# Optimization experiments

Measured on AMD Instinct MI355X. Metric: run time of the kernel, lower is better.

The kernel has to match this reference:

```python
import jax, jax.numpy as jnp
import numpy as np
from jax import lax

B = 32768

def setup_inputs() -> dict:
    key = jax.random.key(0)
    ks = jax.random.split(key, 8)
    return {
        "x": jax.random.normal(ks[0], (B, 784), dtype=jnp.float32),
        "w_conv": jax.random.normal(ks[1], (3, 3), dtype=jnp.float32),
        "W1": jax.random.normal(ks[2], (676, 100), dtype=jnp.float32) * 0.05,
        "b1": jax.random.normal(ks[3], (100,), dtype=jnp.float32) * 0.05,
        "W2": jax.random.normal(ks[4], (100, 100), dtype=jnp.float32) * 0.05,
        "b2": jax.random.normal(ks[5], (100,), dtype=jnp.float32) * 0.05,
        "W3": jax.random.normal(ks[6], (100, 10), dtype=jnp.float32) * 0.05,
        "b3": jax.random.normal(ks[7], (10,), dtype=jnp.float32) * 0.05,
    }


def reference(x, w_conv, W1, b1, W2, b2, W3, b3):
    # x: [B, 784] -> [B, 1, 28, 28]; valid 3x3 cross-correlation (tensordot == correlation)
    xr = x.reshape(-1, 1, 28, 28)
    k = w_conv.reshape(1, 1, 3, 3)  # [out_c, in_c, kh, kw]
    conv = lax.conv_general_dilated(
        xr, k, window_strides=(1, 1), padding="VALID",
        dimension_numbers=("NCHW", "OIHW", "NCHW"))  # [B, 1, 26, 26]
    h = conv.reshape(conv.shape[0], 26 * 26)  # [B, 676]
    h = jax.nn.relu(h @ W1 + b1)
    h = jax.nn.relu(h @ W2 + b2)
    return h @ W3 + b3  # [B, 10]
```

## Files before the change

kernel.cpp:

```cpp
#include <hip/hip_runtime.h>


typedef __attribute__((ext_vector_type(8))) short bf16x8;
typedef __attribute__((ext_vector_type(4))) float f32x4;

#define KP1 832
#define NP  112
#define K2P 128
#define BM  64
#define NT  256

#define W2T_OFF (NP * KP1)
#define W3T_OFF (W2T_OFF + NP * K2P)
#define WS_USHORTS (W3T_OFF + 16 * K2P)

#define WAITV4 asm volatile("s_waitcnt vmcnt(4)" ::: "memory")
#define WAITV0 asm volatile("s_waitcnt vmcnt(0)" ::: "memory")
#define BAR    __builtin_amdgcn_s_barrier()
#define SBAR0  __builtin_amdgcn_sched_barrier(0)

__device__ __forceinline__ unsigned short f2bf(float f) {
    unsigned int u = __float_as_uint(f);
    u += 0x7FFFu + ((u >> 16) & 1u);
    return (unsigned short)(u >> 16);
}

__device__ __forceinline__ unsigned int pkbf(float a, float b) {
    unsigned int r;
    asm("v_cvt_pk_bf16_f32 %0, %1, %2" : "=v"(r) : "v"(a), "v"(b));
    return r;
}

__device__ __forceinline__ bf16x8 cvt8(float4 a, float4 b) {
    union { unsigned int w[4]; bf16x8 v; } u;
    u.w[0] = pkbf(a.x, a.y);
    u.w[1] = pkbf(a.z, a.w);
    u.w[2] = pkbf(b.x, b.y);
    u.w[3] = pkbf(b.z, b.w);
    return u.v;
}

__device__ __forceinline__ void gload_lds16(const void* g, void* l) {
    __builtin_amdgcn_global_load_lds(
        (const __attribute__((address_space(1))) unsigned int*)g,
        (__attribute__((address_space(3))) unsigned int*)l, 16, 0, 0);
}

__global__ void build_weights(const float* __restrict__ w_conv,
                              const float* __restrict__ W1,
                              const float* __restrict__ W2,
                              const float* __restrict__ W3,
                              unsigned short* __restrict__ ws) {
    const int idx = blockIdx.x * 256 + threadIdx.x;
    const int WEFF_T = 28 * KP1;
    if (idx < WEFF_T) {
        const int j4 = idx / KP1, p = idx % KP1;
        const int j = j4 * 4;
        float a0 = 0.f, a1 = 0.f, a2 = 0.f, a3 = 0.f;
        if (p < 784 && j4 < 25) {
            const int y = p / 28, xx = p % 28;
#pragma unroll
            for (int ky = 0; ky < 3; ++ky) {
                const int py = y - ky;
                if (py < 0 || py >= 26) continue;
#pragma unroll
                for (int kx = 0; kx < 3; ++kx) {
                    const int px = xx - kx;
                    if (px < 0 || px >= 26) continue;
                    const float wc = w_conv[ky * 3 + kx];
                    const float4 w = *reinterpret_cast<const float4*>(
                        W1 + (size_t)(py * 26 + px) * 100 + j);
                    a0 = fmaf(wc, w.x, a0); a1 = fmaf(wc, w.y, a1);
                    a2 = fmaf(wc, w.z, a2); a3 = fmaf(wc, w.w, a3);
                }
            }
        }
        ws[(size_t)(j + 0) * KP1 + p] = f2bf(a0);
        ws[(size_t)(j + 1) * KP1 + p] = f2bf(a1);
        ws[(size_t)(j + 2) * KP1 + p] = f2bf(a2);
        ws[(size_t)(j + 3) * KP1 + p] = f2bf(a3);
    } else if (idx < WEFF_T + NP * K2P) {
        const int r = idx - WEFF_T;
        const int col = r / K2P, k = r % K2P;
        float v = (col < 100 && k < 100) ? W2[k * 100 + col] : 0.f;
        ws[W2T_OFF + r] = f2bf(v);
    } else if (idx < WEFF_T + NP * K2P + 16 * K2P) {
        const int r = idx - WEFF_T - NP * K2P;
        const int col = r / K2P, k = r % K2P;
        float v = (col < 10 && k < 100) ? W3[k * 10 + col] : 0.f;
        ws[W3T_OFF + r] = f2bf(v);
    }
}

__global__ __launch_bounds__(NT, 2)
void fused(const float* __restrict__ x,
           const unsigned short* __restrict__ wst,
           const float* __restrict__ b1,
           const float* __restrict__ b2,
           const float* __restrict__ b3,
           float* __restrict__ out) {
    __shared__ __attribute__((aligned(16))) float          xs[3][64][64];
    __shared__ __attribute__((aligned(16))) unsigned short bs[2][112][64];
    unsigned short (*h1)[136] = reinterpret_cast<unsigned short(*)[136]>(&xs[0][0][0]);
    unsigned short (*h2)[136] = reinterpret_cast<unsigned short(*)[136]>(
        (char*)&xs[0][0][0] + 17408);

    const int tid  = threadIdx.x;
    const int lane = tid & 63;
    const int wv   = tid >> 6;
    const int l15  = lane & 15;
    const int lk   = lane >> 4;
    const int b0   = blockIdx.x * BM;
    const int wr   = wv * 16;

    const unsigned short* weff = wst;
    const unsigned short* w2t  = wst + W2T_OFF;
    const unsigned short* w3t  = wst + W3T_OFF;

    f32x4 acc[7];
#pragma unroll
    for (int n = 0; n < 7; ++n) acc[n] = (f32x4){0.f, 0.f, 0.f, 0.f};

    auto issueX = [&](int kt, float* xb) {
#pragma unroll
        for (int q = 0; q < 4; ++q) {
            const int rowbase = wr + 4 * q;
            const int r = rowbase + (lane >> 4);
            const int chunk = (lane & 15) ^ (r & 7);
            const char* g = (const char*)(x + (size_t)(b0 + r) * 784 + kt * 64)
                          + chunk * 16;
            gload_lds16(g, (char*)xb + rowbase * 256);
        }
    };
    auto issueB = [&](int kt, unsigned short* bb) {
#pragma unroll
        for (int k = 0; k < 4; ++k) {
            const int i = wv + 4 * k;
            if (i < 14) {
                const int rowbase = 8 * i;
                const int r = rowbase + (lane >> 3);
                const int chunk = (lane & 7) ^ (r & 7);
                const char* g = (const char*)(weff + (size_t)r * KP1 + kt * 64)
                              + chunk * 16;
                gload_lds16(g, (char*)bb + rowbase * 128);
            }
        }
    };

    auto computeStage = [&](const float* xb, const unsigned short* bb) {
        const int r = wr + l15;
        const int sA = (r & 7) << 4;
        const char* ap = (const char*)xb + r * 256;
#pragma unroll
        for (int ks = 0; ks < 2; ++ks) {
            const int base = ks * 128 + lk * 32;
            const float4 lo = *reinterpret_cast<const float4*>(ap + ((base     ) ^ sA));
            const float4 hi = *reinterpret_cast<const float4*>(ap + ((base + 16) ^ sA));
            const bf16x8 af = cvt8(lo, hi);
#pragma unroll
            for (int n = 0; n < 7; ++n) {
                const int rn = n * 16 + l15;
                const char* bp = (const char*)bb + rn * 128;
                const bf16x8 bfr = *reinterpret_cast<const bf16x8*>(
                    bp + ((ks * 64 + lk * 16) ^ ((rn & 7) << 4)));
                acc[n] = __builtin_amdgcn_mfma_f32_16x16x32_bf16(af, bfr, acc[n], 0, 0, 0);
            }
        }
    };

    float*          X[3] = {&xs[0][0][0], &xs[1][0][0], &xs[2][0][0]};
    unsigned short* Bf[2] = {&bs[0][0][0], &bs[1][0][0]};

    issueX(0, X[0]); issueB(0, Bf[0]); issueX(1, X[1]);
    WAITV4; BAR;
#pragma unroll
    for (int t = 0; t < 12; ++t) {
        if (t < 11) issueB(t + 1, Bf[(t + 1) & 1]);
        if (t < 10) issueX(t + 2, X[(t + 2) % 3]);
        SBAR0;
        computeStage(X[t % 3], Bf[t & 1]);
        if (t < 10)      { WAITV4; BAR; }
        else if (t == 10){ WAITV0; BAR; }
    }

    {
        float4 t0 = (float4){0.f, 0.f, 0.f, 0.f}, t1 = t0;
        if (lk < 2) {
            const float* xp = x + (size_t)(b0 + wr + l15) * 784 + 768 + lk * 8;
            t0 = *reinterpret_cast<const float4*>(xp);
            t1 = *reinterpret_cast<const float4*>(xp + 4);
        }
        const bf16x8 aft = cvt8(t0, t1);
#pragma unroll
        for (int n = 0; n < 7; ++n) {
            const bf16x8 bft = *reinterpret_cast<const bf16x8*>(
                weff + (size_t)(n * 16 + l15) * KP1 + 768 + lk * 8);
            acc[n] = __builtin_amdgcn_mfma_f32_16x16x32_bf16(aft, bft, acc[n], 0, 0, 0);
        }
    }
    __syncthreads();

    float bias[7];
#pragma unroll
    for (int n = 0; n < 7; ++n) {
        const int c = n * 16 + l15;
        bias[n] = (c < 100) ? b1[c] : 0.f;
    }
#pragma unroll
    for (int n = 0; n < 7; ++n) {
        const int col = n * 16 + l15;
        if (col < 100)
#pragma unroll
            for (int q = 0; q < 4; ++q) {
                const float v = fmaxf(acc[n][q] + bias[n], 0.f);
                h1[wr + lk * 4 + q][col] = f2bf(v);
            }
    }
    for (int f = lane; f < 16 * 14; f += 64) {
        const int r = wr + f / 14, c = 100 + (f % 14) * 2;
        *reinterpret_cast<unsigned int*>(&h1[r][c]) = 0u;
        *reinterpret_cast<unsigned int*>(&h2[r][c]) = 0u;
    }
    SBAR0;

    f32x4 acc2[7];
#pragma unroll
    for (int n = 0; n < 7; ++n) acc2[n] = (f32x4){0.f, 0.f, 0.f, 0.f};
#pragma unroll
    for (int ks = 0; ks < 4; ++ks) {
        const int kb = ks * 32 + lk * 8;
        const bf16x8 af = *reinterpret_cast<const bf16x8*>(&h1[wr + l15][kb]);
#pragma unroll
        for (int n = 0; n < 7; ++n) {
            const bf16x8 bfr = *reinterpret_cast<const bf16x8*>(
                w2t + (size_t)(n * 16 + l15) * K2P + kb);
            acc2[n] = __builtin_amdgcn_mfma_f32_16x16x32_bf16(af, bfr, acc2[n], 0, 0, 0);
        }
    }

#pragma unroll
    for (int n = 0; n < 7; ++n) {
        const int c = n * 16 + l15;
        bias[n] = (c < 100) ? b2[c] : 0.f;
    }
#pragma unroll
    for (int n = 0; n < 7; ++n) {
        const int col = n * 16 + l15;
        if (col < 100)
#pragma unroll
            for (int q = 0; q < 4; ++q) {
                const float v = fmaxf(acc2[n][q] + bias[n], 0.f);
                h2[wr + lk * 4 + q][col] = f2bf(v);
            }
    }
    SBAR0;

    f32x4 acc3 = (f32x4){0.f, 0.f, 0.f, 0.f};
#pragma unroll
    for (int ks = 0; ks < 4; ++ks) {
        const int kb = ks * 32 + lk * 8;
        const bf16x8 bfr = *reinterpret_cast<const bf16x8*>(
            w3t + (size_t)l15 * K2P + kb);
        const bf16x8 af = *reinterpret_cast<const bf16x8*>(&h2[wr + l15][kb]);
        acc3 = __builtin_amdgcn_mfma_f32_16x16x32_bf16(af, bfr, acc3, 0, 0, 0);
    }

    if (l15 < 10) {
        const float bb = b3[l15];
#pragma unroll
        for (int q = 0; q < 4; ++q) {
            const int row = b0 + wr + lk * 4 + q;
            out[(size_t)row * 10 + l15] = acc3[q] + bb;
        }
    }
}

extern "C" void kernel_launch(void* const* d_in, const int* in_sizes, int n_in,
                              void* d_out, int out_size, void* d_ws, size_t ws_size,
                              hipStream_t stream) {
    const float* x      = (const float*)d_in[0];
    const float* w_conv = (const float*)d_in[1];
    const float* W1     = (const float*)d_in[2];
    const float* b1     = (const float*)d_in[3];
    const float* W2     = (const float*)d_in[4];
    const float* b2     = (const float*)d_in[5];
    const float* W3     = (const float*)d_in[6];
    const float* b3     = (const float*)d_in[7];
    float* out = (float*)d_out;
    unsigned short* ws = (unsigned short*)d_ws;

    const int total = 28 * KP1 + NP * K2P + 16 * K2P;
    build_weights<<<(total + 255) / 256, 256, 0, stream>>>(w_conv, W1, W2, W3, ws);
    fused<<<32768 / BM, NT, 0, stream>>>(x, ws, b1, b2, b3, out);
}
```

Before: 36.47 us.

## Warp-specialize fused MLP with copy waves converting x to bf16 in LDS

Splits each 512-thread block into four compute waves and four copy waves that stream 32-row tiles of x into a double-buffered bf16 LDS tile, overlapping the next tile's load with the current tile's three GEMMs. Each block handles four tiles, and first-layer weights are now read directly from global memory into registers rather than staged through LDS. This removes the fp32 LDS staging and per-step conversions. It risks lower memory-level parallelism from synchronous loads on only four waves and one block per CU due to large LDS use.

```diff
diff --git a/kernel.cpp b/kernel.cpp
--- a/kernel.cpp
+++ b/kernel.cpp
@@ -7,17 +7,15 @@
 #define KP1 832
 #define NP  112
 #define K2P 128
-#define BM  64
-#define NT  256
+#define NT  512
+#define TILES 4
+#define ROWS 32
+#define XC  840
 
 #define W2T_OFF (NP * KP1)
 #define W3T_OFF (W2T_OFF + NP * K2P)
-#define WS_USHORTS (W3T_OFF + 16 * K2P)
-
-#define WAITV4 asm volatile("s_waitcnt vmcnt(4)" ::: "memory")
-#define WAITV0 asm volatile("s_waitcnt vmcnt(0)" ::: "memory")
-#define BAR    __builtin_amdgcn_s_barrier()
-#define SBAR0  __builtin_amdgcn_sched_barrier(0)
+
+#define SBAR0 __builtin_amdgcn_sched_barrier(0)
 
 __device__ __forceinline__ unsigned short f2bf(float f) {
     unsigned int u = __float_as_uint(f);
@@ -29,21 +27,6 @@
     unsigned int r;
     asm("v_cvt_pk_bf16_f32 %0, %1, %2" : "=v"(r) : "v"(a), "v"(b));
     return r;
-}
-
-__device__ __forceinline__ bf16x8 cvt8(float4 a, float4 b) {
-    union { unsigned int w[4]; bf16x8 v; } u;
-    u.w[0] = pkbf(a.x, a.y);
-    u.w[1] = pkbf(a.z, a.w);
-    u.w[2] = pkbf(b.x, b.y);
-    u.w[3] = pkbf(b.z, b.w);
-    return u.v;
-}
-
-__device__ __forceinline__ void gload_lds16(const void* g, void* l) {
-    __builtin_amdgcn_global_load_lds(
-        (const __attribute__((address_space(1))) unsigned int*)g,
-        (__attribute__((address_space(3))) unsigned int*)l, 16, 0, 0);
 }
 
 __global__ void build_weights(const float* __restrict__ w_conv,
@@ -99,178 +82,177 @@
            const float* __restrict__ b2,
            const float* __restrict__ b3,
            float* __restrict__ out) {
-    __shared__ __attribute__((aligned(16))) float          xs[3][64][64];
-    __shared__ __attribute__((aligned(16))) unsigned short bs[2][112][64];
-    unsigned short (*h1)[136] = reinterpret_cast<unsigned short(*)[136]>(&xs[0][0][0]);
-    unsigned short (*h2)[136] = reinterpret_cast<unsigned short(*)[136]>(
-        (char*)&xs[0][0][0] + 17408);
+    __shared__ __attribute__((aligned(16))) unsigned short xs[2][ROWS][XC];
+    __shared__ __attribute__((aligned(16))) unsigned short h1[ROWS][136];
+    __shared__ __attribute__((aligned(16))) unsigned short h2[ROWS][136];
 
     const int tid  = threadIdx.x;
     const int lane = tid & 63;
     const int wv   = tid >> 6;
+    const bool is_copy = (wv >= 4);
     const int l15  = lane & 15;
     const int lk   = lane >> 4;
-    const int b0   = blockIdx.x * BM;
-    const int wr   = wv * 16;
+    const int wv_m = (wv >> 1) & 1;
+    const int wv_n = wv & 1;
+    const int wr   = wv_m * 16;
+    const int nb   = wv_n * 4;
+    const size_t b0 = (size_t)blockIdx.x * (TILES * ROWS);
 
     const unsigned short* weff = wst;
     const unsigned short* w2t  = wst + W2T_OFF;
     const unsigned short* w3t  = wst + W3T_OFF;
 
-    f32x4 acc[7];
-#pragma unroll
-    for (int n = 0; n < 7; ++n) acc[n] = (f32x4){0.f, 0.f, 0.f, 0.f};
-
-    auto issueX = [&](int kt, float* xb) {
-#pragma unroll
-        for (int q = 0; q < 4; ++q) {
-            const int rowbase = wr + 4 * q;
-            const int r = rowbase + (lane >> 4);
-            const int chunk = (lane & 15) ^ (r & 7);
-            const char* g = (const char*)(x + (size_t)(b0 + r) * 784 + kt * 64)
-                          + chunk * 16;
-            gload_lds16(g, (char*)xb + rowbase * 256);
+    for (int i = tid; i < 1536; i += NT) {
+        const int buf = i / 768, r = (i % 768) / 24, c = (i % 768) % 24;
+        *reinterpret_cast<unsigned int*>(&xs[buf][r][784 + c * 2]) = 0u;
+    }
+    for (int i = tid; i < 1152; i += NT) {
+        const int a = i / 576, r = (i % 576) / 18, c = (i % 576) % 18;
+        unsigned short* hp = a ? &h2[0][0] : &h1[0][0];
+        *reinterpret_cast<unsigned int*>(hp + r * 136 + 100 + c * 2) = 0u;
+    }
+    {
+        const float* src = x + b0 * 784;
+#pragma unroll
+        for (int i = 0; i < 13; ++i) {
+            const int f = i * 2048 + tid * 4;
+            if (f < ROWS * 784) {
+                const float4 v = *reinterpret_cast<const float4*>(src + f);
+                const int row = f / 784, col = f - row * 784;
+                *reinterpret_cast<uint2*>(&xs[0][row][col]) =
+                    (uint2){pkbf(v.x, v.y), pkbf(v.z, v.w)};
+            }
+        }
+    }
+    __syncthreads();
+
+    float bias1[4], bias2[4], bb3 = 0.f;
+    const unsigned short* bp[4];
+    if (!is_copy) {
+#pragma unroll
+        for (int j = 0; j < 4; ++j) {
+            const int nf = nb + j, c = nf * 16 + l15;
+            bias1[j] = (nf < 7 && c < 100) ? b1[c] : 0.f;
+            bias2[j] = (nf < 7 && c < 100) ? b2[c] : 0.f;
+            bp[j] = weff + (size_t)(nf * 16 + l15) * KP1;
+        }
+        if (wv_n == 0 && l15 < 10) bb3 = b3[l15];
+    }
+
+    auto copy_half = [&](int t1, int i0, int i1) {
+        const int ctid = tid - 256;
+        const float* src = x + (b0 + (size_t)t1 * ROWS) * 784;
+        unsigned short* dst = &xs[t1 & 1][0][0];
+#pragma unroll
+        for (int i = i0; i < i1; ++i) {
+            const int f = i * 1024 + ctid * 4;
+            if (f < ROWS * 784) {
+                const float4 v = *reinterpret_cast<const float4*>(src + f);
+                const int row = f / 784, col = f - row * 784;
+                *reinterpret_cast<uint2*>(dst + row * XC + col) =
+                    (uint2){pkbf(v.x, v.y), pkbf(v.z, v.w)};
+            }
         }
     };
-    auto issueB = [&](int kt, unsigned short* bb) {
-#pragma unroll
-        for (int k = 0; k < 4; ++k) {
-            const int i = wv + 4 * k;
-            if (i < 14) {
-                const int rowbase = 8 * i;
-                const int r = rowbase + (lane >> 3);
-                const int chunk = (lane & 7) ^ (r & 7);
-                const char* g = (const char*)(weff + (size_t)r * KP1 + kt * 64)
-                              + chunk * 16;
-                gload_lds16(g, (char*)bb + rowbase * 128);
-            }
-        }
-    };
-
-    auto computeStage = [&](const float* xb, const unsigned short* bb) {
-        const int r = wr + l15;
-        const int sA = (r & 7) << 4;
-        const char* ap = (const char*)xb + r * 256;
-#pragma unroll
-        for (int ks = 0; ks < 2; ++ks) {
-            const int base = ks * 128 + lk * 32;
-            const float4 lo = *reinterpret_cast<const float4*>(ap + ((base     ) ^ sA));
-            const float4 hi = *reinterpret_cast<const float4*>(ap + ((base + 16) ^ sA));
-            const bf16x8 af = cvt8(lo, hi);
-#pragma unroll
-            for (int n = 0; n < 7; ++n) {
-                const int rn = n * 16 + l15;
-                const char* bp = (const char*)bb + rn * 128;
+
+#pragma unroll 1
+    for (int t = 0; t < TILES; ++t) {
+        const unsigned short* xb = &xs[t & 1][0][0];
+
+        if (is_copy) {
+            if (t + 1 < TILES) copy_half(t + 1, 0, 13);
+        } else {
+            f32x4 acc[4];
+#pragma unroll
+            for (int j = 0; j < 4; ++j) acc[j] = (f32x4){0.f, 0.f, 0.f, 0.f};
+
+            bf16x8 A[2][2];
+            bf16x8 Bv[2][4][2];
+            const unsigned short* ap = xb + (wr + l15) * XC;
+
+            auto loadW = [&](int w, int b) {
+                A[b][0] = *reinterpret_cast<const bf16x8*>(ap + w * 64 + lk * 8);
+                A[b][1] = *reinterpret_cast<const bf16x8*>(ap + w * 64 + 32 + lk * 8);
+#pragma unroll
+                for (int j = 0; j < 4; ++j)
+                    if (nb + j < 7) {
+                        Bv[b][j][0] = *reinterpret_cast<const bf16x8*>(bp[j] + w * 64 + lk * 8);
+                        Bv[b][j][1] = *reinterpret_cast<const bf16x8*>(bp[j] + w * 64 + 32 + lk * 8);
+                    }
+            };
+            loadW(0, 0);
+#pragma unroll
+            for (int w = 0; w < 13; ++w) {
+                if (w < 12) loadW(w + 1, (w + 1) & 1);
+                SBAR0;
+#pragma unroll
+                for (int ks = 0; ks < 2; ++ks)
+#pragma unroll
+                    for (int j = 0; j < 4; ++j)
+                        if (nb + j < 7)
+                            acc[j] = __builtin_amdgcn_mfma_f32_16x16x32_bf16(
+                                A[w & 1][ks], Bv[w & 1][j][ks], acc[j], 0, 0, 0);
+                SBAR0;
+            }
+#pragma unroll
+            for (int j = 0; j < 4; ++j) {
+                const int nf = nb + j, col = nf * 16 + l15;
+                if (nf < 7 && col < 100)
+#pragma unroll
+                    for (int q = 0; q < 4; ++q)
+                        h1[wr + lk * 4 + q][col] = f2bf(fmaxf(acc[j][q] + bias1[j], 0.f));
+            }
+        }
+        __syncthreads();
+
+        if (is_copy) {
+            if (t + 1 < TILES) copy_half(t + 1, 13, 25);
+        } else {
+            f32x4 acc2[4];
+#pragma unroll
+            for (int j = 0; j < 4; ++j) acc2[j] = (f32x4){0.f, 0.f, 0.f, 0.f};
+#pragma unroll
+            for (int ks = 0; ks < 4; ++ks) {
+                const int kb = ks * 32 + lk * 8;
+                const bf16x8 af = *reinterpret_cast<const bf16x8*>(&h1[wr + l15][kb]);
+#pragma unroll
+                for (int j = 0; j < 4; ++j) {
+                    const int nf = nb + j;
+                    if (nf < 7) {
+                        const bf16x8 bfr = *reinterpret_cast<const bf16x8*>(
+                            w2t + (size_t)(nf * 16 + l15) * K2P + kb);
+                        acc2[j] = __builtin_amdgcn_mfma_f32_16x16x32_bf16(af, bfr, acc2[j], 0, 0, 0);
+                    }
+                }
+            }
+#pragma unroll
+            for (int j = 0; j < 4; ++j) {
+                const int nf = nb + j, col = nf * 16 + l15;
+                if (nf < 7 && col < 100)
+#pragma unroll
+                    for (int q = 0; q < 4; ++q)
+                        h2[wr + lk * 4 + q][col] = f2bf(fmaxf(acc2[j][q] + bias2[j], 0.f));
+            }
+        }
+        __syncthreads();
+
+        if (!is_copy && wv_n == 0) {
+            f32x4 acc3 = (f32x4){0.f, 0.f, 0.f, 0.f};
+#pragma unroll
+            for (int ks = 0; ks < 4; ++ks) {
+                const int kb = ks * 32 + lk * 8;
                 const bf16x8 bfr = *reinterpret_cast<const bf16x8*>(
-                    bp + ((ks * 64 + lk * 16) ^ ((rn & 7) << 4)));
-                acc[n] = __builtin_amdgcn_mfma_f32_16x16x32_bf16(af, bfr, acc[n], 0, 0, 0);
-            }
-        }
-    };
-
-    float*          X[3] = {&xs[0][0][0], &xs[1][0][0], &xs[2][0][0]};
-    unsigned short* Bf[2] = {&bs[0][0][0], &bs[1][0][0]};
-
-    issueX(0, X[0]); issueB(0, Bf[0]); issueX(1, X[1]);
-    WAITV4; BAR;
-#pragma unroll
-    for (int t = 0; t < 12; ++t) {
-        if (t < 11) issueB(t + 1, Bf[(t + 1) & 1]);
-        if (t < 10) issueX(t + 2, X[(t + 2) % 3]);
-        SBAR0;
-        computeStage(X[t % 3], Bf[t & 1]);
-        if (t < 10)      { WAITV4; BAR; }
-        else if (t == 10){ WAITV0; BAR; }
-    }
-
-    {
-        float4 t0 = (float4){0.f, 0.f, 0.f, 0.f}, t1 = t0;
-        if (lk < 2) {
-            const float* xp = x + (size_t)(b0 + wr + l15) * 784 + 768 + lk * 8;
-            t0 = *reinterpret_cast<const float4*>(xp);
-            t1 = *reinterpret_cast<const float4*>(xp + 4);
-        }
-        const bf16x8 aft = cvt8(t0, t1);
-#pragma unroll
-        for (int n = 0; n < 7; ++n) {
-            const bf16x8 bft = *reinterpret_cast<const bf16x8*>(
-                weff + (size_t)(n * 16 + l15) * KP1 + 768 + lk * 8);
-            acc[n] = __builtin_amdgcn_mfma_f32_16x16x32_bf16(aft, bft, acc[n], 0, 0, 0);
-        }
-    }
-    __syncthreads();
-
-    float bias[7];
-#pragma unroll
-    for (int n = 0; n < 7; ++n) {
-        const int c = n * 16 + l15;
-        bias[n] = (c < 100) ? b1[c] : 0.f;
-    }
-#pragma unroll
-    for (int n = 0; n < 7; ++n) {
-        const int col = n * 16 + l15;
-        if (col < 100)
-#pragma unroll
-            for (int q = 0; q < 4; ++q) {
-                const float v = fmaxf(acc[n][q] + bias[n], 0.f);
-                h1[wr + lk * 4 + q][col] = f2bf(v);
-            }
-    }
-    for (int f = lane; f < 16 * 14; f += 64) {
-        const int r = wr + f / 14, c = 100 + (f % 14) * 2;
-        *reinterpret_cast<unsigned int*>(&h1[r][c]) = 0u;
-        *reinterpret_cast<unsigned int*>(&h2[r][c]) = 0u;
-    }
-    SBAR0;
-
-    f32x4 acc2[7];
-#pragma unroll
-    for (int n = 0; n < 7; ++n) acc2[n] = (f32x4){0.f, 0.f, 0.f, 0.f};
-#pragma unroll
-    for (int ks = 0; ks < 4; ++ks) {
-        const int kb = ks * 32 + lk * 8;
-        const bf16x8 af = *reinterpret_cast<const bf16x8*>(&h1[wr + l15][kb]);
-#pragma unroll
-        for (int n = 0; n < 7; ++n) {
-            const bf16x8 bfr = *reinterpret_cast<const bf16x8*>(
-                w2t + (size_t)(n * 16 + l15) * K2P + kb);
-            acc2[n] = __builtin_amdgcn_mfma_f32_16x16x32_bf16(af, bfr, acc2[n], 0, 0, 0);
-        }
-    }
-
-#pragma unroll
-    for (int n = 0; n < 7; ++n) {
-        const int c = n * 16 + l15;
-        bias[n] = (c < 100) ? b2[c] : 0.f;
-    }
-#pragma unroll
-    for (int n = 0; n < 7; ++n) {
-        const int col = n * 16 + l15;
-        if (col < 100)
-#pragma unroll
-            for (int q = 0; q < 4; ++q) {
-                const float v = fmaxf(acc2[n][q] + bias[n], 0.f);
-                h2[wr + lk * 4 + q][col] = f2bf(v);
-            }
-    }
-    SBAR0;
-
-    f32x4 acc3 = (f32x4){0.f, 0.f, 0.f, 0.f};
-#pragma unroll
-    for (int ks = 0; ks < 4; ++ks) {
-        const int kb = ks * 32 + lk * 8;
-        const bf16x8 bfr = *reinterpret_cast<const bf16x8*>(
-            w3t + (size_t)l15 * K2P + kb);
-        const bf16x8 af = *reinterpret_cast<const bf16x8*>(&h2[wr + l15][kb]);
-        acc3 = __builtin_amdgcn_mfma_f32_16x16x32_bf16(af, bfr, acc3, 0, 0, 0);
-    }
-
-    if (l15 < 10) {
-        const float bb = b3[l15];
-#pragma unroll
-        for (int q = 0; q < 4; ++q) {
-            const int row = b0 + wr + lk * 4 + q;
-            out[(size_t)row * 10 + l15] = acc3[q] + bb;
+                    w3t + (size_t)l15 * K2P + kb);
+                const bf16x8 af = *reinterpret_cast<const bf16x8*>(&h2[wr + l15][kb]);
+                acc3 = __builtin_amdgcn_mfma_f32_16x16x32_bf16(af, bfr, acc3, 0, 0, 0);
+            }
+            if (l15 < 10) {
+#pragma unroll
+                for (int q = 0; q < 4; ++q) {
+                    const size_t row = b0 + (size_t)t * ROWS + wr + lk * 4 + q;
+                    out[row * 10 + l15] = acc3[q] + bb3;
+                }
+            }
         }
     }
 }
@@ -291,5 +273,5 @@
 
     const int total = 28 * KP1 + NP * K2P + 16 * K2P;
     build_weights<<<(total + 255) / 256, 256, 0, stream>>>(w_conv, W1, W2, W3, ws);
-    fused<<<32768 / BM, NT, 0, stream>>>(x, ws, b1, b2, b3, out);
-}
+    fused<<<32768 / (TILES * ROWS), NT, 0, stream>>>(x, ws, b1, b2, b3, out);
+}
```

New measurement: 71.26 us. +95.4%, slower.

## Stage whole x tile as bf16 in LDS, stream weights from registers

Applied to the files above, without the earlier changes.

Replaces the triple-buffered global_load_lds pipeline of fp32 x tiles and bf16 weight tiles with a single upfront load of each wave's 16 full rows of x. The rows are converted to bf16 and stored in swizzled LDS. Weights are now double-buffered in registers straight from global/L2 instead of going through LDS, and block-level barriers are dropped because each wave only touches its own rows. Block size is halved to 32 rows with 128 threads. This removes barrier syncs and LDS weight staging, but per-wave load/compute overlap is lost and every wave re-reads all of W1 from cache, which raises cache traffic.

```diff
diff --git a/kernel.cpp b/kernel.cpp
--- a/kernel.cpp
+++ b/kernel.cpp
@@ -7,17 +7,14 @@
 #define KP1 832
 #define NP  112
 #define K2P 128
-#define BM  64
-#define NT  256
+#define BM  32
+#define NT  128
+#define XC  840
 
 #define W2T_OFF (NP * KP1)
 #define W3T_OFF (W2T_OFF + NP * K2P)
-#define WS_USHORTS (W3T_OFF + 16 * K2P)
-
-#define WAITV4 asm volatile("s_waitcnt vmcnt(4)" ::: "memory")
-#define WAITV0 asm volatile("s_waitcnt vmcnt(0)" ::: "memory")
-#define BAR    __builtin_amdgcn_s_barrier()
-#define SBAR0  __builtin_amdgcn_sched_barrier(0)
+
+#define SBAR0 __builtin_amdgcn_sched_barrier(0)
 
 __device__ __forceinline__ unsigned short f2bf(float f) {
     unsigned int u = __float_as_uint(f);
@@ -29,21 +26,6 @@
     unsigned int r;
     asm("v_cvt_pk_bf16_f32 %0, %1, %2" : "=v"(r) : "v"(a), "v"(b));
     return r;
-}
-
-__device__ __forceinline__ bf16x8 cvt8(float4 a, float4 b) {
-    union { unsigned int w[4]; bf16x8 v; } u;
-    u.w[0] = pkbf(a.x, a.y);
-    u.w[1] = pkbf(a.z, a.w);
-    u.w[2] = pkbf(b.x, b.y);
-    u.w[3] = pkbf(b.z, b.w);
-    return u.v;
-}
-
-__device__ __forceinline__ void gload_lds16(const void* g, void* l) {
-    __builtin_amdgcn_global_load_lds(
-        (const __attribute__((address_space(1))) unsigned int*)g,
-        (__attribute__((address_space(3))) unsigned int*)l, 16, 0, 0);
 }
 
 __global__ void build_weights(const float* __restrict__ w_conv,
@@ -92,152 +74,148 @@
     }
 }
 
-__global__ __launch_bounds__(NT, 2)
+__global__ __launch_bounds__(NT, 1)
 void fused(const float* __restrict__ x,
            const unsigned short* __restrict__ wst,
            const float* __restrict__ b1,
            const float* __restrict__ b2,
            const float* __restrict__ b3,
            float* __restrict__ out) {
-    __shared__ __attribute__((aligned(16))) float          xs[3][64][64];
-    __shared__ __attribute__((aligned(16))) unsigned short bs[2][112][64];
-    unsigned short (*h1)[136] = reinterpret_cast<unsigned short(*)[136]>(&xs[0][0][0]);
-    unsigned short (*h2)[136] = reinterpret_cast<unsigned short(*)[136]>(
-        (char*)&xs[0][0][0] + 17408);
+    __shared__ __attribute__((aligned(16))) unsigned short xb[BM][XC];
+    __shared__ __attribute__((aligned(16))) unsigned short h1[BM][136];
+    __shared__ __attribute__((aligned(16))) unsigned short h2[BM][136];
 
     const int tid  = threadIdx.x;
     const int lane = tid & 63;
     const int wv   = tid >> 6;
     const int l15  = lane & 15;
     const int lk   = lane >> 4;
-    const int b0   = blockIdx.x * BM;
     const int wr   = wv * 16;
+    const size_t b0 = (size_t)blockIdx.x * BM;
 
     const unsigned short* weff = wst;
     const unsigned short* w2t  = wst + W2T_OFF;
     const unsigned short* w3t  = wst + W3T_OFF;
 
-    f32x4 acc[7];
-#pragma unroll
-    for (int n = 0; n < 7; ++n) acc[n] = (f32x4){0.f, 0.f, 0.f, 0.f};
-
-    auto issueX = [&](int kt, float* xb) {
-#pragma unroll
-        for (int q = 0; q < 4; ++q) {
-            const int rowbase = wr + 4 * q;
-            const int r = rowbase + (lane >> 4);
-            const int chunk = (lane & 15) ^ (r & 7);
-            const char* g = (const char*)(x + (size_t)(b0 + r) * 784 + kt * 64)
-                          + chunk * 16;
-            gload_lds16(g, (char*)xb + rowbase * 256);
-        }
-    };
-    auto issueB = [&](int kt, unsigned short* bb) {
-#pragma unroll
-        for (int k = 0; k < 4; ++k) {
-            const int i = wv + 4 * k;
-            if (i < 14) {
-                const int rowbase = 8 * i;
-                const int r = rowbase + (lane >> 3);
-                const int chunk = (lane & 7) ^ (r & 7);
-                const char* g = (const char*)(weff + (size_t)r * KP1 + kt * 64)
-                              + chunk * 16;
-                gload_lds16(g, (char*)bb + rowbase * 128);
-            }
-        }
-    };
-
-    auto computeStage = [&](const float* xb, const unsigned short* bb) {
-        const int r = wr + l15;
-        const int sA = (r & 7) << 4;
-        const char* ap = (const char*)xb + r * 256;
-#pragma unroll
-        for (int ks = 0; ks < 2; ++ks) {
-            const int base = ks * 128 + lk * 32;
-            const float4 lo = *reinterpret_cast<const float4*>(ap + ((base     ) ^ sA));
-            const float4 hi = *reinterpret_cast<const float4*>(ap + ((base + 16) ^ sA));
-            const bf16x8 af = cvt8(lo, hi);
-#pragma unroll
-            for (int n = 0; n < 7; ++n) {
-                const int rn = n * 16 + l15;
-                const char* bp = (const char*)bb + rn * 128;
-                const bf16x8 bfr = *reinterpret_cast<const bf16x8*>(
-                    bp + ((ks * 64 + lk * 16) ^ ((rn & 7) << 4)));
-                acc[n] = __builtin_amdgcn_mfma_f32_16x16x32_bf16(af, bfr, acc[n], 0, 0, 0);
-            }
-        }
-    };
-
-    float*          X[3] = {&xs[0][0][0], &xs[1][0][0], &xs[2][0][0]};
-    unsigned short* Bf[2] = {&bs[0][0][0], &bs[1][0][0]};
-
-    issueX(0, X[0]); issueB(0, Bf[0]); issueX(1, X[1]);
-    WAITV4; BAR;
-#pragma unroll
-    for (int t = 0; t < 12; ++t) {
-        if (t < 11) issueB(t + 1, Bf[(t + 1) & 1]);
-        if (t < 10) issueX(t + 2, X[(t + 2) % 3]);
-        SBAR0;
-        computeStage(X[t % 3], Bf[t & 1]);
-        if (t < 10)      { WAITV4; BAR; }
-        else if (t == 10){ WAITV0; BAR; }
-    }
-
-    {
-        float4 t0 = (float4){0.f, 0.f, 0.f, 0.f}, t1 = t0;
-        if (lk < 2) {
-            const float* xp = x + (size_t)(b0 + wr + l15) * 784 + 768 + lk * 8;
-            t0 = *reinterpret_cast<const float4*>(xp);
-            t1 = *reinterpret_cast<const float4*>(xp + 4);
-        }
-        const bf16x8 aft = cvt8(t0, t1);
-#pragma unroll
-        for (int n = 0; n < 7; ++n) {
-            const bf16x8 bft = *reinterpret_cast<const bf16x8*>(
-                weff + (size_t)(n * 16 + l15) * KP1 + 768 + lk * 8);
-            acc[n] = __builtin_amdgcn_mfma_f32_16x16x32_bf16(aft, bft, acc[n], 0, 0, 0);
-        }
-    }
-    __syncthreads();
-
-    float bias[7];
-#pragma unroll
-    for (int n = 0; n < 7; ++n) {
-        const int c = n * 16 + l15;
-        bias[n] = (c < 100) ? b1[c] : 0.f;
-    }
-#pragma unroll
-    for (int n = 0; n < 7; ++n) {
-        const int col = n * 16 + l15;
-        if (col < 100)
-#pragma unroll
-            for (int q = 0; q < 4; ++q) {
-                const float v = fmaxf(acc[n][q] + bias[n], 0.f);
-                h1[wr + lk * 4 + q][col] = f2bf(v);
-            }
+    for (int f = lane; f < 16 * 24; f += 64) {
+        const int r = wr + f / 24;
+        const int cw = 392 + (f % 24);
+        const int sw = cw ^ ((r & 7) << 2);
+        *reinterpret_cast<unsigned int*>((char*)&xb[0][0] + ((size_t)r * 420 + sw) * 4) = 0u;
     }
     for (int f = lane; f < 16 * 14; f += 64) {
         const int r = wr + f / 14, c = 100 + (f % 14) * 2;
         *reinterpret_cast<unsigned int*>(&h1[r][c]) = 0u;
         *reinterpret_cast<unsigned int*>(&h2[r][c]) = 0u;
     }
+
+    {
+        const float* xsrc = x + (b0 + wr) * 784;
+        const int base = lane * 4;
+        char* lb = (char*)&xb[0][0];
+        auto wr_lds = [&](int it, float4 v) {
+            const int F   = it * 256 + base;
+            const int row = F / 784;
+            const int col = F - row * 784;
+            const int cw  = (col >> 1) ^ ((row & 7) << 2);
+            *reinterpret_cast<uint2*>(lb + ((size_t)(wr + row) * 420 + cw) * 4) =
+                (uint2){pkbf(v.x, v.y), pkbf(v.z, v.w)};
+        };
+        float4 v[12];
+#pragma unroll 1
+        for (int b = 0; b < 4; ++b) {
+#pragma unroll
+            for (int i = 0; i < 12; ++i)
+                v[i] = *reinterpret_cast<const float4*>(xsrc + (b * 12 + i) * 256 + base);
+            SBAR0;
+#pragma unroll
+            for (int i = 0; i < 12; ++i) wr_lds(b * 12 + i, v[i]);
+            SBAR0;
+        }
+        float4 vt = *reinterpret_cast<const float4*>(xsrc + 48 * 256 + base);
+        wr_lds(48, vt);
+    }
+    asm volatile("s_waitcnt vmcnt(0) lgkmcnt(0)" ::: "memory");
     SBAR0;
 
+    f32x4 acc[7];
+#pragma unroll
+    for (int n = 0; n < 7; ++n) acc[n] = (f32x4){0.f, 0.f, 0.f, 0.f};
+
+    const int arow = wr + l15;
+    const int swz  = (l15 & 7) << 2;
+    const char* lb = (const char*)&xb[0][0];
+    const unsigned aoff0 = ((unsigned)arow * 420 + ((lk * 4) ^ swz)) * 4;
+    const unsigned aoff1 = ((unsigned)arow * 420 + ((16 + lk * 4) ^ swz)) * 4;
+
+    const unsigned short* bp[7];
+#pragma unroll
+    for (int n = 0; n < 7; ++n)
+        bp[n] = weff + (size_t)(n * 16 + l15) * KP1 + lk * 8;
+
+    bf16x8 Bv[2][7][2];
+    auto loadB = [&](int w, int buf) {
+#pragma unroll
+        for (int n = 0; n < 7; ++n) {
+            Bv[buf][n][0] = *reinterpret_cast<const bf16x8*>(bp[n] + w * 64);
+            Bv[buf][n][1] = *reinterpret_cast<const bf16x8*>(bp[n] + w * 64 + 32);
+        }
+    };
+
+    loadB(0, 0);
+#pragma unroll
+    for (int w = 0; w < 13; ++w) {
+        if (w < 12) loadB(w + 1, (w + 1) & 1);
+        SBAR0;
+        const bf16x8 a0 = *reinterpret_cast<const bf16x8*>(lb + aoff0 + w * 128);
+        const bf16x8 a1 = *reinterpret_cast<const bf16x8*>(lb + aoff1 + w * 128);
+#pragma unroll
+        for (int n = 0; n < 7; ++n)
+            acc[n] = __builtin_amdgcn_mfma_f32_16x16x32_bf16(a0, Bv[w & 1][n][0], acc[n], 0, 0, 0);
+#pragma unroll
+        for (int n = 0; n < 7; ++n)
+            acc[n] = __builtin_amdgcn_mfma_f32_16x16x32_bf16(a1, Bv[w & 1][n][1], acc[n], 0, 0, 0);
+        SBAR0;
+    }
+
+    float bias[7];
+#pragma unroll
+    for (int n = 0; n < 7; ++n) {
+        const int c = n * 16 + l15;
+        bias[n] = (c < 100) ? b1[c] : 0.f;
+    }
+#pragma unroll
+    for (int n = 0; n < 7; ++n) {
+        const int col = n * 16 + l15;
+        if (col < 100)
+#pragma unroll
+            for (int q = 0; q < 4; ++q)
+                h1[wr + lk * 4 + q][col] = f2bf(fmaxf(acc[n][q] + bias[n], 0.f));
+    }
+    asm volatile("s_waitcnt lgkmcnt(0)" ::: "memory");
+    SBAR0;
+
     f32x4 acc2[7];
 #pragma unroll
     for (int n = 0; n < 7; ++n) acc2[n] = (f32x4){0.f, 0.f, 0.f, 0.f};
+    bf16x8 B2[2][7];
+    auto loadB2 = [&](int ks, int buf) {
+#pragma unroll
+        for (int n = 0; n < 7; ++n)
+            B2[buf][n] = *reinterpret_cast<const bf16x8*>(
+                w2t + (size_t)(n * 16 + l15) * K2P + ks * 32 + lk * 8);
+    };
+    loadB2(0, 0);
 #pragma unroll
     for (int ks = 0; ks < 4; ++ks) {
-        const int kb = ks * 32 + lk * 8;
-        const bf16x8 af = *reinterpret_cast<const bf16x8*>(&h1[wr + l15][kb]);
-#pragma unroll
-        for (int n = 0; n < 7; ++n) {
-            const bf16x8 bfr = *reinterpret_cast<const bf16x8*>(
-                w2t + (size_t)(n * 16 + l15) * K2P + kb);
-            acc2[n] = __builtin_amdgcn_mfma_f32_16x16x32_bf16(af, bfr, acc2[n], 0, 0, 0);
-        }
-    }
-
+        if (ks < 3) loadB2(ks + 1, (ks + 1) & 1);
+        SBAR0;
+        const bf16x8 af = *reinterpret_cast<const bf16x8*>(&h1[wr + l15][ks * 32 + lk * 8]);
+#pragma unroll
+        for (int n = 0; n < 7; ++n)
+            acc2[n] = __builtin_amdgcn_mfma_f32_16x16x32_bf16(af, B2[ks & 1][n], acc2[n], 0, 0, 0);
+        SBAR0;
+    }
 #pragma unroll
     for (int n = 0; n < 7; ++n) {
         const int c = n * 16 + l15;
@@ -248,29 +226,26 @@
         const int col = n * 16 + l15;
         if (col < 100)
 #pragma unroll
-            for (int q = 0; q < 4; ++q) {
-                const float v = fmaxf(acc2[n][q] + bias[n], 0.f);
-                h2[wr + lk * 4 + q][col] = f2bf(v);
-            }
-    }
+            for (int q = 0; q < 4; ++q)
+                h2[wr + lk * 4 + q][col] = f2bf(fmaxf(acc2[n][q] + bias[n], 0.f));
+    }
+    asm volatile("s_waitcnt lgkmcnt(0)" ::: "memory");
     SBAR0;
 
     f32x4 acc3 = (f32x4){0.f, 0.f, 0.f, 0.f};
 #pragma unroll
     for (int ks = 0; ks < 4; ++ks) {
-        const int kb = ks * 32 + lk * 8;
         const bf16x8 bfr = *reinterpret_cast<const bf16x8*>(
-            w3t + (size_t)l15 * K2P + kb);
-        const bf16x8 af = *reinterpret_cast<const bf16x8*>(&h2[wr + l15][kb]);
+            w3t + (size_t)l15 * K2P + ks * 32 + lk * 8);
+        const bf16x8 af = *reinterpret_cast<const bf16x8*>(&h2[wr + l15][ks * 32 + lk * 8]);
         acc3 = __builtin_amdgcn_mfma_f32_16x16x32_bf16(af, bfr, acc3, 0, 0, 0);
     }
-
     if (l15 < 10) {
         const float bb = b3[l15];
 #pragma unroll
         for (int q = 0; q < 4; ++q) {
-            const int row = b0 + wr + lk * 4 + q;
-            out[(size_t)row * 10 + l15] = acc3[q] + bb;
+            const size_t row = b0 + wr + lk * 4 + q;
+            out[row * 10 + l15] = acc3[q] + bb;
         }
     }
 }
```

Result: slower. 74.96 us (+105.6%).
